# Optimization experiments

Hardware: AMD Instinct MI355X
Metric: run time of the kernel (lower is better)

Reference implementation:

```python
import jax, jax.numpy as jnp
import numpy as np

B, S, D, H = 2, 2048, 1024, 16
HD = D // H  # head_dim = 64


def setup_inputs() -> dict:
    key = jax.random.key(0)
    ks = jax.random.split(key, 6)
    sc = 1.0 / np.sqrt(D)
    x = jax.random.normal(ks[0], (B, S, D), dtype=jnp.float32)
    # causal boolean mask, broadcast over heads: [B, 1, S, S]
    causal = jnp.tril(jnp.ones((S, S), dtype=bool))
    attn_mask = jnp.broadcast_to(causal[None, None], (B, 1, S, S))
    return {
        "x": x,
        "attn_mask": attn_mask,
        "Wq": jax.random.normal(ks[1], (D, D), dtype=jnp.float32) * sc,
        "bq": jnp.zeros((D,), dtype=jnp.float32),
        "Wk": jax.random.normal(ks[2], (D, D), dtype=jnp.float32) * sc,
        "bk": jnp.zeros((D,), dtype=jnp.float32),
        "Wv": jax.random.normal(ks[3], (D, D), dtype=jnp.float32) * sc,
        "bv": jnp.zeros((D,), dtype=jnp.float32),
        "Wo": jax.random.normal(ks[4], (D, D), dtype=jnp.float32) * sc,
        "bo": jnp.zeros((D,), dtype=jnp.float32),
    }


def _split_heads(t):
    # [B, S, D] -> [B, H, S, HD]
    return t.reshape(B, S, H, HD).transpose(0, 2, 1, 3)


def reference(x, attn_mask, Wq, bq, Wk, bk, Wv, bv, Wo, bo):
    q = _split_heads(x @ Wq + bq)
    k = _split_heads(x @ Wk + bk)
    v = _split_heads(x @ Wv + bv)
    scale = 1.0 / jnp.sqrt(jnp.asarray(HD, dtype=x.dtype))
    # [B, H, S, S] scores
    scores = jnp.einsum("bhqd,bhkd->bhqk", q, k) * scale
    scores = jnp.where(attn_mask, scores, jnp.asarray(-jnp.inf, dtype=x.dtype))
    probs = jax.nn.softmax(scores, axis=-1)
    out = jnp.einsum("bhqk,bhkd->bhqd", probs, v)  # [B, H, S, HD]
    out = out.transpose(0, 2, 1, 3).reshape(B, S, D)
    return out @ Wo + bo
```

## Files before the change

kernel.cpp:

```cpp
#include <hip/hip_runtime.h>
#include <math.h>

#define BB 2
#define SS 2048
#define DDIM 1024
#define HH 16
#define HD 64
#define MM (BB * SS)

typedef short s16x8 __attribute__((ext_vector_type(8)));
typedef short s16x4 __attribute__((ext_vector_type(4)));
typedef float f32x4 __attribute__((ext_vector_type(4)));
typedef unsigned int u32x4 __attribute__((ext_vector_type(4)));

__device__ __forceinline__ unsigned short f2bf(float f) {
    unsigned int u = __builtin_bit_cast(unsigned int, f);
    u += 0x7fffu + ((u >> 16) & 1u);
    return (unsigned short)(u >> 16);
}
__device__ __forceinline__ float bf2f(unsigned short h) {
    return __builtin_bit_cast(float, (unsigned int)h << 16);
}

template <int MODE>
__global__ __launch_bounds__(256) void proj_gemm(
    const float* __restrict__ A, const float* __restrict__ W,
    const float* __restrict__ bias, void* __restrict__ Cout)
{
    __shared__ short Bh[128][64];
    __shared__ short Bl[128][64];

    const int tid  = threadIdx.x;
    const int lane = tid & 63;
    const int wave = tid >> 6;
    const int g    = lane >> 4;
    const int qq   = lane & 15;
    const int wm   = (wave >> 1) * 64;
    const int wn   = (wave & 1) * 64;
    const int n0   = blockIdx.x * 128;
    const int m0   = blockIdx.y * 128;

    f32x4 acc[4][4];
#pragma unroll
    for (int i = 0; i < 4; ++i)
#pragma unroll
        for (int j = 0; j < 4; ++j) acc[i][j] = (f32x4){0.f, 0.f, 0.f, 0.f};

    for (int kt = 0; kt < 16; ++kt) {
        const int k0 = kt * 64;
        __syncthreads();
#pragma unroll
        for (int uu = 0; uu < 2; ++uu) {
            const int u  = tid + uu * 256;
            const int kg = u >> 5;
            const int nb = u & 31;
#pragma unroll
            for (int j = 0; j < 4; ++j) {
                const int n = nb + 32 * j;
                float v[4];
#pragma unroll
                for (int i = 0; i < 4; ++i)
                    v[i] = W[(size_t)(k0 + 4 * kg + i) * DDIM + n0 + n];
                short h4[4], l4[4];
#pragma unroll
                for (int i = 0; i < 4; ++i) {
                    const unsigned short hh = f2bf(v[i]);
                    h4[i] = (short)hh;
                    l4[i] = (short)f2bf(v[i] - bf2f(hh));
                }
                const s16x4 hv = {h4[0], h4[1], h4[2], h4[3]};
                const s16x4 lv = {l4[0], l4[1], l4[2], l4[3]};
                const int slot = (kg >> 1) ^ (n & 7);
                const int half = kg & 1;
                *(s16x4*)((char*)&Bh[0][0] + n * 128 + slot * 16 + half * 8) = hv;
                *(s16x4*)((char*)&Bl[0][0] + n * 128 + slot * 16 + half * 8) = lv;
            }
        }
        __syncthreads();

#pragma unroll
        for (int ks = 0; ks < 2; ++ks) {
            s16x8 bhf[4], blf[4];
#pragma unroll
            for (int nf = 0; nf < 4; ++nf) {
                const int n = wn + 16 * nf + qq;
                const int pslot = (4 * ks + g) ^ (n & 7);
                bhf[nf] = *(const s16x8*)((const char*)&Bh[0][0] + n * 128 + pslot * 16);
                blf[nf] = *(const s16x8*)((const char*)&Bl[0][0] + n * 128 + pslot * 16);
            }
#pragma unroll
            for (int mf = 0; mf < 4; ++mf) {
                const float* ap = &A[(size_t)(m0 + wm + 16 * mf + qq) * DDIM + k0 + ks * 32 + g * 8];
                const float4 a0 = *(const float4*)ap;
                const float4 a1 = *(const float4*)(ap + 4);
                float av[8] = {a0.x, a0.y, a0.z, a0.w, a1.x, a1.y, a1.z, a1.w};
                s16x8 ah, al;
#pragma unroll
                for (int i = 0; i < 8; ++i) {
                    const unsigned short hh = f2bf(av[i]);
                    ah[i] = (short)hh;
                    al[i] = (short)f2bf(av[i] - bf2f(hh));
                }
#pragma unroll
                for (int nf = 0; nf < 4; ++nf) {
                    acc[mf][nf] = __builtin_amdgcn_mfma_f32_16x16x32_bf16(ah, bhf[nf], acc[mf][nf], 0, 0, 0);
                    acc[mf][nf] = __builtin_amdgcn_mfma_f32_16x16x32_bf16(ah, blf[nf], acc[mf][nf], 0, 0, 0);
                    acc[mf][nf] = __builtin_amdgcn_mfma_f32_16x16x32_bf16(al, bhf[nf], acc[mf][nf], 0, 0, 0);
                }
            }
        }
    }

    float bv[4];
#pragma unroll
    for (int nf = 0; nf < 4; ++nf) bv[nf] = bias[n0 + wn + 16 * nf + qq];

#pragma unroll
    for (int mf = 0; mf < 4; ++mf) {
#pragma unroll
        for (int nf = 0; nf < 4; ++nf) {
            const int ncol = n0 + wn + 16 * nf + qq;
            if (MODE == 2) {
                const int mbase = m0 + wm + 16 * mf + 4 * g;
                const int b = mbase >> 11, s = mbase & 2047;
                const int h = ncol >> 6, d = ncol & 63;
                short p4[4];
#pragma unroll
                for (int r = 0; r < 4; ++r)
                    p4[r] = (short)f2bf(acc[mf][nf][r] + bv[nf]);
                const s16x4 pv = {p4[0], p4[1], p4[2], p4[3]};
                *(s16x4*)&((short*)Cout)[(((size_t)(b * HH + h)) * HD + d) * SS + s] = pv;
            } else {
#pragma unroll
                for (int r = 0; r < 4; ++r) {
                    const int mrow = m0 + wm + 16 * mf + 4 * g + r;
                    const float val = acc[mf][nf][r] + bv[nf];
                    if (MODE == 3) {
                        ((float*)Cout)[(size_t)mrow * DDIM + ncol] = val;
                    } else {
                        const int b = mrow >> 11, s = mrow & 2047;
                        const int h = ncol >> 6, d = ncol & 63;
                        if (MODE == 0) {
                            short* Q = (short*)Cout;
                            const size_t base = (((size_t)(b * HH + h)) * SS + s) * 128;
                            const unsigned short hh = f2bf(val);
                            Q[base + d]      = (short)hh;
                            Q[base + 64 + d] = (short)f2bf(val - bf2f(hh));
                        } else {
                            ((short*)Cout)[(((size_t)(b * HH + h)) * SS + s) * 64 + d] = (short)f2bf(val);
                        }
                    }
                }
            }
        }
    }
}

__global__ __launch_bounds__(256) void attn_mfma(
    const short* __restrict__ Qp, const short* __restrict__ Kp,
    const short* __restrict__ Vt, float* __restrict__ Ab)
{
    __shared__ short Kt[64 * 64];
    __shared__ short Vs[64 * 64];

    const int tid  = threadIdx.x;
    const int lane = tid & 63;
    const int wave = tid >> 6;
    const int g    = lane >> 4;
    const int qq   = lane & 15;
    const int qt   = 31 - blockIdx.x;
    const int h    = blockIdx.y;
    const int b    = blockIdx.z;
    const int q0   = qt * 64;
    const int qrow = q0 + wave * 16 + qq;

    const size_t headoff = (size_t)(b * HH + h) * SS;

    s16x8 qf[2][2];
#pragma unroll
    for (int half = 0; half < 2; ++half)
#pragma unroll
        for (int ks2 = 0; ks2 < 2; ++ks2)
            qf[half][ks2] = *(const s16x8*)&Qp[(headoff + qrow) * 128 + half * 64 + ks2 * 32 + g * 8];

    f32x4 oacc[4];
#pragma unroll
    for (int i = 0; i < 4; ++i) oacc[i] = (f32x4){0.f, 0.f, 0.f, 0.f};
    float mrun = -INFINITY, lrun = 0.f;

    for (int kt = 0; kt <= qt; ++kt) {
        const int kc0 = kt * 64;
        __syncthreads();
#pragma unroll
        for (int uu = 0; uu < 2; ++uu) {
            const int S = uu * 256 + tid;
            const int row = S >> 3, sl = S & 7;
            const int dsl = (sl ^ (row & 7)) * 8;
            const s16x8 kv = *(const s16x8*)&Kp[(headoff + kc0 + row) * 64 + sl * 8];
            *(s16x8*)&Kt[row * 64 + dsl] = kv;
            const s16x8 vv = *(const s16x8*)&Vt[((size_t)(b * HH + h) * HD + row) * SS + kc0 + sl * 8];
            *(s16x8*)&Vs[row * 64 + dsl] = vv;
        }
        __syncthreads();

        f32x4 sacc[4];
#pragma unroll
        for (int i = 0; i < 4; ++i) sacc[i] = (f32x4){0.f, 0.f, 0.f, 0.f};
#pragma unroll
        for (int kcf = 0; kcf < 4; ++kcf) {
            const int row = kcf * 16 + qq;
            s16x8 kf[2];
#pragma unroll
            for (int ks2 = 0; ks2 < 2; ++ks2)
                kf[ks2] = *(const s16x8*)&Kt[row * 64 + (((ks2 * 4 + g) ^ (row & 7)) * 8)];
#pragma unroll
            for (int half = 0; half < 2; ++half)
#pragma unroll
                for (int ks2 = 0; ks2 < 2; ++ks2)
                    sacc[kcf] = __builtin_amdgcn_mfma_f32_16x16x32_bf16(kf[ks2], qf[half][ks2], sacc[kcf], 0, 0, 0);
        }

        float sc[16];
        float pmax = -INFINITY;
#pragma unroll
        for (int kcf = 0; kcf < 4; ++kcf)
#pragma unroll
            for (int r = 0; r < 4; ++r) {
                float v = sacc[kcf][r] * 0.125f;
                const int kc = kc0 + kcf * 16 + g * 4 + r;
                if (kc > qrow) v = -INFINITY;
                sc[kcf * 4 + r] = v;
                pmax = fmaxf(pmax, v);
            }
        pmax = fmaxf(pmax, __shfl_xor(pmax, 16));
        pmax = fmaxf(pmax, __shfl_xor(pmax, 32));
        const float mnew  = fmaxf(mrun, pmax);
        const float alpha = __expf(mrun - mnew);
        float p[16], psum = 0.f;
#pragma unroll
        for (int i = 0; i < 16; ++i) { p[i] = __expf(sc[i] - mnew); psum += p[i]; }
        psum += __shfl_xor(psum, 16);
        psum += __shfl_xor(psum, 32);
        lrun = lrun * alpha + psum;
        mrun = mnew;
#pragma unroll
        for (int df = 0; df < 4; ++df) oacc[df] *= alpha;

        unsigned int pk[4][2];
#pragma unroll
        for (int kcf = 0; kcf < 4; ++kcf)
#pragma unroll
            for (int hh = 0; hh < 2; ++hh)
                pk[kcf][hh] = (unsigned int)f2bf(p[kcf * 4 + 2 * hh]) |
                              ((unsigned int)f2bf(p[kcf * 4 + 2 * hh + 1]) << 16);

        s16x8 pb[2];
#pragma unroll
        for (int ks = 0; ks < 2; ++ks) {
            unsigned int w_[4];
#pragma unroll
            for (int w = 0; w < 2 * 2; ++w) {
                const int gs  = (2 * g + (w >> 1)) & 3;
                const int src = qq | (gs << 4);
                const unsigned int va = (unsigned int)__shfl((int)pk[2 * ks][w & 1], src);
                const unsigned int vb = (unsigned int)__shfl((int)pk[2 * ks + 1][w & 1], src);
                w_[w] = (g & 2) ? vb : va;
            }
            const u32x4 t = {w_[0], w_[1], w_[2], w_[3]};
            pb[ks] = __builtin_bit_cast(s16x8, t);
        }

#pragma unroll
        for (int df = 0; df < 4; ++df) {
            const int row = df * 16 + qq;
#pragma unroll
            for (int ks = 0; ks < 2; ++ks) {
                const s16x8 vf = *(const s16x8*)&Vs[row * 64 + (((ks * 4 + g) ^ (row & 7)) * 8)];
                oacc[df] = __builtin_amdgcn_mfma_f32_16x16x32_bf16(vf, pb[ks], oacc[df], 0, 0, 0);
            }
        }
    }

    const float inv = 1.0f / lrun;
#pragma unroll
    for (int df = 0; df < 4; ++df) {
        f32x4 r = oacc[df];
        r *= inv;
        *(f32x4*)&Ab[((size_t)b * SS + qrow) * DDIM + h * HD + df * 16 + g * 4] = r;
    }
}

extern "C" void kernel_launch(void* const* d_in, const int* in_sizes, int n_in,
                              void* d_out, int out_size, void* d_ws, size_t ws_size,
                              hipStream_t stream)
{
    const float* x  = (const float*)d_in[0];
    const float* Wq = (const float*)d_in[2];
    const float* bq = (const float*)d_in[3];
    const float* Wk = (const float*)d_in[4];
    const float* bk = (const float*)d_in[5];
    const float* Wv = (const float*)d_in[6];
    const float* bv = (const float*)d_in[7];
    const float* Wo = (const float*)d_in[8];
    const float* bo = (const float*)d_in[9];
    float* out = (float*)d_out;

    char* w = (char*)d_ws;
    short* Qp = (short*)w;
    short* Kp = (short*)(w + (size_t)16 * 1024 * 1024);
    short* Vt = (short*)(w + (size_t)24 * 1024 * 1024);
    float* Ab = (float*)(w + (size_t)32 * 1024 * 1024);

    const dim3 blk(256);
    const dim3 gg(DDIM / 128, MM / 128);

    proj_gemm<0><<<gg, blk, 0, stream>>>(x, Wq, bq, (void*)Qp);
    proj_gemm<1><<<gg, blk, 0, stream>>>(x, Wk, bk, (void*)Kp);
    proj_gemm<2><<<gg, blk, 0, stream>>>(x, Wv, bv, (void*)Vt);

    attn_mfma<<<dim3(32, HH, BB), blk, 0, stream>>>(Qp, Kp, Vt, Ab);

    proj_gemm<3><<<gg, blk, 0, stream>>>(Ab, Wo, bo, (void*)out);
}
```

Measured before the change: 568.6 us.

## Pre-split weights into transposed bf16 hi/lo once and shrink GEMM tiles

Adds a wsplit kernel that transposes all four weight matrices and splits each into bf16 high and low parts once per call. The projection GEMM then loads pre-split 16-byte vectors straight into swizzled LDS instead of doing strided fp32 loads and conversions per tile. Tiles shrink from 128x128 to 64x64 to raise the block count, and Q is staged in the output buffer to free workspace. This costs an extra kernel launch and weight traffic, and the smaller tiles reduce data reuse per block.

After: 498.4 us. -12.4%, faster.

```diff
diff --git a/kernel.cpp b/kernel.cpp
--- a/kernel.cpp
+++ b/kernel.cpp
@@ -22,78 +22,109 @@
     return __builtin_bit_cast(float, (unsigned int)h << 16);
 }
 
+__global__ __launch_bounds__(256) void wsplit(
+    const float* __restrict__ W0, const float* __restrict__ W1,
+    const float* __restrict__ W2, const float* __restrict__ W3,
+    short* __restrict__ WtH, short* __restrict__ WtL)
+{
+    __shared__ float T[64][65];
+    const int z  = blockIdx.z;
+    const float* W = (z == 0) ? W0 : (z == 1) ? W1 : (z == 2) ? W2 : W3;
+    const int n0 = blockIdx.x * 64;
+    const int k0 = blockIdx.y * 64;
+    const int t  = threadIdx.x;
+
+#pragma unroll
+    for (int i = 0; i < 4; ++i) {
+        const int kr = (t >> 4) + i * 16;
+        const int c4 = (t & 15) * 4;
+        const float4 v = *(const float4*)&W[(size_t)(k0 + kr) * DDIM + n0 + c4];
+        T[kr][c4 + 0] = v.x; T[kr][c4 + 1] = v.y;
+        T[kr][c4 + 2] = v.z; T[kr][c4 + 3] = v.w;
+    }
+    __syncthreads();
+
+    const int n  = t >> 2;
+    const int kb = (t & 3) * 16;
+    s16x8 h0, h1, l0, l1;
+#pragma unroll
+    for (int j = 0; j < 8; ++j) {
+        const float f0 = T[kb + j][n];
+        const unsigned short hh0 = f2bf(f0);
+        h0[j] = (short)hh0; l0[j] = (short)f2bf(f0 - bf2f(hh0));
+        const float f1 = T[kb + 8 + j][n];
+        const unsigned short hh1 = f2bf(f1);
+        h1[j] = (short)hh1; l1[j] = (short)f2bf(f1 - bf2f(hh1));
+    }
+    const size_t ob = ((size_t)z * DDIM + n0 + n) * DDIM + k0 + kb;
+    *(s16x8*)&WtH[ob]     = h0;
+    *(s16x8*)&WtH[ob + 8] = h1;
+    *(s16x8*)&WtL[ob]     = l0;
+    *(s16x8*)&WtL[ob + 8] = l1;
+}
+
 template <int MODE>
-__global__ __launch_bounds__(256) void proj_gemm(
-    const float* __restrict__ A, const float* __restrict__ W,
-    const float* __restrict__ bias, void* __restrict__ Cout)
+__global__ __launch_bounds__(256) void proj_v2(
+    const float* __restrict__ A, const short* __restrict__ BTh,
+    const short* __restrict__ BTl, const float* __restrict__ bias,
+    void* __restrict__ Cout)
 {
-    __shared__ short Bh[128][64];
-    __shared__ short Bl[128][64];
+    __shared__ short Bh[64 * 64];
+    __shared__ short Bl[64 * 64];
 
     const int tid  = threadIdx.x;
     const int lane = tid & 63;
     const int wave = tid >> 6;
     const int g    = lane >> 4;
     const int qq   = lane & 15;
-    const int wm   = (wave >> 1) * 64;
-    const int wn   = (wave & 1) * 64;
-    const int n0   = blockIdx.x * 128;
-    const int m0   = blockIdx.y * 128;
-
-    f32x4 acc[4][4];
-#pragma unroll
-    for (int i = 0; i < 4; ++i)
-#pragma unroll
-        for (int j = 0; j < 4; ++j) acc[i][j] = (f32x4){0.f, 0.f, 0.f, 0.f};
+    const int wm   = (wave >> 1) * 32;
+    const int wn   = (wave & 1) * 32;
+    const int n0   = blockIdx.x * 64;
+    const int m0   = blockIdx.y * 64;
+
+    const int sr = tid >> 2;
+    const int sc = (tid & 3) * 2;
+    const int d0 = sr * 64 + ((sc ^ (sr & 7)) * 8);
+    const int d1 = sr * 64 + (((sc + 1) ^ (sr & 7)) * 8);
+
+    f32x4 acc[2][2];
+#pragma unroll
+    for (int i = 0; i < 2; ++i)
+#pragma unroll
+        for (int j = 0; j < 2; ++j) acc[i][j] = (f32x4){0.f, 0.f, 0.f, 0.f};
 
     for (int kt = 0; kt < 16; ++kt) {
         const int k0 = kt * 64;
         __syncthreads();
-#pragma unroll
-        for (int uu = 0; uu < 2; ++uu) {
-            const int u  = tid + uu * 256;
-            const int kg = u >> 5;
-            const int nb = u & 31;
-#pragma unroll
-            for (int j = 0; j < 4; ++j) {
-                const int n = nb + 32 * j;
-                float v[4];
-#pragma unroll
-                for (int i = 0; i < 4; ++i)
-                    v[i] = W[(size_t)(k0 + 4 * kg + i) * DDIM + n0 + n];
-                short h4[4], l4[4];
-#pragma unroll
-                for (int i = 0; i < 4; ++i) {
-                    const unsigned short hh = f2bf(v[i]);
-                    h4[i] = (short)hh;
-                    l4[i] = (short)f2bf(v[i] - bf2f(hh));
-                }
-                const s16x4 hv = {h4[0], h4[1], h4[2], h4[3]};
-                const s16x4 lv = {l4[0], l4[1], l4[2], l4[3]};
-                const int slot = (kg >> 1) ^ (n & 7);
-                const int half = kg & 1;
-                *(s16x4*)((char*)&Bh[0][0] + n * 128 + slot * 16 + half * 8) = hv;
-                *(s16x4*)((char*)&Bl[0][0] + n * 128 + slot * 16 + half * 8) = lv;
-            }
+        {
+            const size_t gb = (size_t)(n0 + sr) * DDIM + k0 + sc * 8;
+            const s16x8 h0 = *(const s16x8*)&BTh[gb];
+            const s16x8 h1 = *(const s16x8*)&BTh[gb + 8];
+            const s16x8 l0 = *(const s16x8*)&BTl[gb];
+            const s16x8 l1 = *(const s16x8*)&BTl[gb + 8];
+            *(s16x8*)&Bh[d0] = h0;
+            *(s16x8*)&Bh[d1] = h1;
+            *(s16x8*)&Bl[d0] = l0;
+            *(s16x8*)&Bl[d1] = l1;
         }
         __syncthreads();
 
 #pragma unroll
         for (int ks = 0; ks < 2; ++ks) {
-            s16x8 bhf[4], blf[4];
-#pragma unroll
-            for (int nf = 0; nf < 4; ++nf) {
-                const int n = wn + 16 * nf + qq;
-                const int pslot = (4 * ks + g) ^ (n & 7);
-                bhf[nf] = *(const s16x8*)((const char*)&Bh[0][0] + n * 128 + pslot * 16);
-                blf[nf] = *(const s16x8*)((const char*)&Bl[0][0] + n * 128 + pslot * 16);
-            }
-#pragma unroll
-            for (int mf = 0; mf < 4; ++mf) {
+            s16x8 bhf[2], blf[2];
+#pragma unroll
+            for (int nf = 0; nf < 2; ++nf) {
+                const int r  = wn + 16 * nf + qq;
+                const int ch = (((ks * 4 + g) ^ (qq & 7)) * 8);
+                bhf[nf] = *(const s16x8*)&Bh[r * 64 + ch];
+                blf[nf] = *(const s16x8*)&Bl[r * 64 + ch];
+            }
+#pragma unroll
+            for (int mf = 0; mf < 2; ++mf) {
                 const float* ap = &A[(size_t)(m0 + wm + 16 * mf + qq) * DDIM + k0 + ks * 32 + g * 8];
                 const float4 a0 = *(const float4*)ap;
                 const float4 a1 = *(const float4*)(ap + 4);
-                float av[8] = {a0.x, a0.y, a0.z, a0.w, a1.x, a1.y, a1.z, a1.w};
+                const float av[8] = {a0.x, a0.y, a0.z, a0.w, a1.x, a1.y, a1.z, a1.w};
                 s16x8 ah, al;
 #pragma unroll
                 for (int i = 0; i < 8; ++i) {
@@ -102,7 +133,7 @@
                     al[i] = (short)f2bf(av[i] - bf2f(hh));
                 }
 #pragma unroll
-                for (int nf = 0; nf < 4; ++nf) {
+                for (int nf = 0; nf < 2; ++nf) {
                     acc[mf][nf] = __builtin_amdgcn_mfma_f32_16x16x32_bf16(ah, bhf[nf], acc[mf][nf], 0, 0, 0);
                     acc[mf][nf] = __builtin_amdgcn_mfma_f32_16x16x32_bf16(ah, blf[nf], acc[mf][nf], 0, 0, 0);
                     acc[mf][nf] = __builtin_amdgcn_mfma_f32_16x16x32_bf16(al, bhf[nf], acc[mf][nf], 0, 0, 0);
@@ -111,14 +142,14 @@
         }
     }
 
-    float bv[4];
-#pragma unroll
-    for (int nf = 0; nf < 4; ++nf) bv[nf] = bias[n0 + wn + 16 * nf + qq];
-
-#pragma unroll
-    for (int mf = 0; mf < 4; ++mf) {
-#pragma unroll
-        for (int nf = 0; nf < 4; ++nf) {
+    float bv2[2];
+#pragma unroll
+    for (int nf = 0; nf < 2; ++nf) bv2[nf] = bias[n0 + wn + 16 * nf + qq];
+
+#pragma unroll
+    for (int mf = 0; mf < 2; ++mf) {
+#pragma unroll
+        for (int nf = 0; nf < 2; ++nf) {
             const int ncol = n0 + wn + 16 * nf + qq;
             if (MODE == 2) {
                 const int mbase = m0 + wm + 16 * mf + 4 * g;
@@ -127,14 +158,14 @@
                 short p4[4];
 #pragma unroll
                 for (int r = 0; r < 4; ++r)
-                    p4[r] = (short)f2bf(acc[mf][nf][r] + bv[nf]);
+                    p4[r] = (short)f2bf(acc[mf][nf][r] + bv2[nf]);
                 const s16x4 pv = {p4[0], p4[1], p4[2], p4[3]};
                 *(s16x4*)&((short*)Cout)[(((size_t)(b * HH + h)) * HD + d) * SS + s] = pv;
             } else {
 #pragma unroll
                 for (int r = 0; r < 4; ++r) {
                     const int mrow = m0 + wm + 16 * mf + 4 * g + r;
-                    const float val = acc[mf][nf][r] + bv[nf];
+                    const float val = acc[mf][nf][r] + bv2[nf];
                     if (MODE == 3) {
                         ((float*)Cout)[(size_t)mrow * DDIM + ncol] = val;
                     } else {
@@ -306,19 +337,23 @@
     float* out = (float*)d_out;
 
     char* w = (char*)d_ws;
-    short* Qp = (short*)w;
-    short* Kp = (short*)(w + (size_t)16 * 1024 * 1024);
-    short* Vt = (short*)(w + (size_t)24 * 1024 * 1024);
-    float* Ab = (float*)(w + (size_t)32 * 1024 * 1024);
+    short* Kp  = (short*)w;
+    short* Vt  = (short*)(w + (size_t) 8 * 1024 * 1024);
+    float* Ab  = (float*)(w + (size_t)16 * 1024 * 1024);
+    short* WtH = (short*)(w + (size_t)32 * 1024 * 1024);
+    short* WtL = (short*)(w + (size_t)40 * 1024 * 1024);
+    short* Qp  = (short*)d_out;
 
     const dim3 blk(256);
-    const dim3 gg(DDIM / 128, MM / 128);
-
-    proj_gemm<0><<<gg, blk, 0, stream>>>(x, Wq, bq, (void*)Qp);
-    proj_gemm<1><<<gg, blk, 0, stream>>>(x, Wk, bk, (void*)Kp);
-    proj_gemm<2><<<gg, blk, 0, stream>>>(x, Wv, bv, (void*)Vt);
+    const dim3 gg(DDIM / 64, MM / 64);
+
+    wsplit<<<dim3(16, 16, 4), blk, 0, stream>>>(Wq, Wk, Wv, Wo, WtH, WtL);
+
+    proj_v2<0><<<gg, blk, 0, stream>>>(x,  WtH + (size_t)0 * 1048576, WtL + (size_t)0 * 1048576, bq, (void*)Qp);
+    proj_v2<1><<<gg, blk, 0, stream>>>(x,  WtH + (size_t)1 * 1048576, WtL + (size_t)1 * 1048576, bk, (void*)Kp);
+    proj_v2<2><<<gg, blk, 0, stream>>>(x,  WtH + (size_t)2 * 1048576, WtL + (size_t)2 * 1048576, bv, (void*)Vt);
 
     attn_mfma<<<dim3(32, HH, BB), blk, 0, stream>>>(Qp, Kp, Vt, Ab);
 
-    proj_gemm<3><<<gg, blk, 0, stream>>>(Ab, Wo, bo, (void*)out);
-}
+    proj_v2<3><<<gg, blk, 0, stream>>>(Ab, WtH + (size_t)3 * 1048576, WtL + (size_t)3 * 1048576, bo, (void*)out);
+}
```
